# Kernel optimization log

Hardware: AMD Instinct MI355X
Metric: run time of the kernel (lower is better)

## Reference

```python
import jax, jax.numpy as jnp
import numpy as np

B = 128        # graphs per batch
N = 512        # nodes per graph (all graphs full-size)
F = 128        # input/hidden feature dim
DEG_AVG = 16   # average degree
E = B * N * DEG_AVG
DEGREES = (3, 3)  # polynomial filter order per conv layer


def setup_inputs() -> dict:
    key = jax.random.key(0)
    ks = jax.random.split(key, 8)
    X = jax.random.normal(ks[0], (B * N, F), dtype=jnp.float32)
    batch = jnp.repeat(jnp.arange(B, dtype=jnp.int32), N)
    # edges constrained within each graph: graph id = e // (N*DEG_AVG)
    gid = jnp.repeat(jnp.arange(B, dtype=jnp.int32), N * DEG_AVG)
    src = jax.random.randint(ks[1], (E,), 0, N, dtype=jnp.int32) + gid * N
    dst = jax.random.randint(ks[2], (E,), 0, N, dtype=jnp.int32) + gid * N
    edge_index = jnp.stack([src, dst], axis=0)
    s = 1.0 / np.sqrt(F)
    W1 = jax.random.normal(ks[3], (F, F), dtype=jnp.float32) * s
    b1 = jnp.zeros((F,), dtype=jnp.float32)
    W2 = jax.random.normal(ks[4], (F, F), dtype=jnp.float32) * s
    b2 = jnp.zeros((F,), dtype=jnp.float32)
    Wr1 = jax.random.normal(ks[5], (F, 64), dtype=jnp.float32) * s
    br1 = jnp.zeros((64,), dtype=jnp.float32)
    Wr2 = jax.random.normal(ks[6], (64, 1), dtype=jnp.float32) * (1.0 / 8.0)
    br2 = jnp.zeros((1,), dtype=jnp.float32)
    return {"X": X, "batch": batch, "edge_index": edge_index,
            "W1": W1, "b1": b1, "W2": W2, "b2": b2,
            "Wr1": Wr1, "br1": br1, "Wr2": Wr2, "br2": br2}


def _build_gso(edge_index):
    # dense per-graph adjacency [B, N, N] (block-diagonal global GSO,
    # represented batched for efficiency)
    g = edge_index[0] // N
    si = edge_index[0] % N
    di = edge_index[1] % N
    A = jnp.zeros((B, N, N), dtype=jnp.float32).at[g, si, di].set(1.0)
    # gso_generator: symmetric degree-normalized adjacency D^-1/2 A D^-1/2
    deg = A.sum(axis=-1)
    dinv = jnp.where(deg > 0, jax.lax.rsqrt(jnp.maximum(deg, 1e-12)), 0.0)
    S = dinv[:, :, None] * A * dinv[:, None, :]
    return S


def _poly_conv(S, x, degree, W, b):
    # sum_{k=0..degree} S^k x, then linear projection
    acc = x
    z = x
    for _ in range(degree):
        z = jnp.einsum('bij,bjf->bif', S, z)
        acc = acc + z
    return jnp.einsum('bnf,fo->bno', acc, W) + b


def reference(X, batch, edge_index, W1, b1, W2, b2, Wr1, br1, Wr2, br2):
    S = _build_gso(edge_index)
    x = X.reshape(B, N, F)  # nodes grouped per graph (batch is sorted)
    x = jax.nn.relu(_poly_conv(S, x, DEGREES[0], W1, b1))
    x = jax.nn.relu(_poly_conv(S, x, DEGREES[1], W2, b2))
    # global mean pool over nodes of each graph
    h = x.mean(axis=1)  # [B, F]
    h = jax.nn.relu(h @ Wr1 + br1)
    out = (h @ Wr2 + br2).squeeze(-1)  # [B]
    return out
```

## Files before the change

kernel.cpp:

```cpp
#include <hip/hip_runtime.h>
#include <hip/hip_bf16.h>

#define NB 128
#define NN 512
#define NF 128
#define BN (NB*NN)
#define NE (BN*16)
#define EPG 8192
#define WPR 16
#define ELLW 64
#define QST 40
#define SST 72
#define WTS 136

typedef short sh8 __attribute__((ext_vector_type(8)));
typedef float f32x4 __attribute__((ext_vector_type(4)));

static __device__ __forceinline__ unsigned short f2bf(float f) {
    unsigned u = __float_as_uint(f);
    u += 0x7fffu + ((u >> 16) & 1u);
    return (unsigned short)(u >> 16);
}

#define DOT2LO(acc_, pk_, one_) \
    asm("v_dot2_f32_bf16 %0, %1, %2, %0" : "+v"(acc_) : "v"(pk_), "v"(one_))

__global__ __launch_bounds__(512) void build_ell_fused_kernel(
    const int* __restrict__ src, const int* __restrict__ dst,
    unsigned short* __restrict__ ell, int* __restrict__ ocnt,
    float* __restrict__ dinvr, int* __restrict__ perm)
{
    __shared__ unsigned bm[NN * WPR];
    __shared__ int cs[NN];
    __shared__ int rdeg[NN];
    __shared__ int irank[NN];
    int g = blockIdx.x;
    int t = threadIdx.x;

    for (int i = t; i < NN * WPR; i += 512) bm[i] = 0u;
    __syncthreads();

    const int4* sg4 = (const int4*)(src + (size_t)g * EPG);
    const int4* dg4 = (const int4*)(dst + (size_t)g * EPG);
    for (int i = t; i < EPG / 4; i += 512) {
        int4 s4 = sg4[i];
        int4 d4 = dg4[i];
        int s, d;
        s = s4.x & (NN - 1); d = d4.x & (NN - 1);
        atomicOr(&bm[s * WPR + (d >> 5)], 1u << (d & 31));
        s = s4.y & (NN - 1); d = d4.y & (NN - 1);
        atomicOr(&bm[s * WPR + (d >> 5)], 1u << (d & 31));
        s = s4.z & (NN - 1); d = d4.z & (NN - 1);
        atomicOr(&bm[s * WPR + (d >> 5)], 1u << (d & 31));
        s = s4.w & (NN - 1); d = d4.w & (NN - 1);
        atomicOr(&bm[s * WPR + (d >> 5)], 1u << (d & 31));
    }
    __syncthreads();

    unsigned rw[WPR];
    #pragma unroll
    for (int w = 0; w < WPR; ++w) rw[w] = bm[t * WPR + w];
    int deg = 0;
    #pragma unroll
    for (int w = 0; w < WPR; ++w) deg += __popc(rw[w]);
    if (deg > ELLW) deg = ELLW;
    cs[t] = deg;
    __syncthreads();

    int rk = 0;
    for (int i = 0; i < NN; ++i) {
        int di_ = cs[i];
        rk += (di_ < deg) || (di_ == deg && i < t);
    }
    rdeg[rk] = deg;
    irank[t] = rk;
    perm[(size_t)g * NN + rk] = t;
    dinvr[(size_t)g * NN + rk] = (deg > 0) ? rsqrtf((float)deg) : 0.0f;
    __syncthreads();

    if (t < NN / 8) {
        int m = rdeg[t * 8 + 7];
        ocnt[(size_t)g * (NN / 8) + t] = (m + 3) & ~3;
    }

    unsigned short* els = (unsigned short*)bm;
    for (int qtr = 0; qtr < 4; ++qtr) {
        if ((rk >> 7) == qtr) {
            unsigned short* er = &els[(rk & 127) * SST];
            int c = 0;
            #pragma unroll
            for (int w = 0; w < WPR; ++w) {
                unsigned bits = rw[w];
                while (bits) {
                    int j = __ffs(bits) - 1;
                    bits &= bits - 1;
                    if (c < ELLW) er[c] = (unsigned short)irank[w * 32 + j];
                    ++c;
                }
            }
            if (c > ELLW) c = ELLW;
            for (int p = c; p < ELLW; ++p) er[p] = (unsigned short)NN;
        }
        __syncthreads();
        unsigned short* outb = ell + ((size_t)g * NN + qtr * 128) * ELLW;
        for (int idx = t; idx < 1024; idx += 512) {
            int r2 = idx >> 3, sg2 = idx & 7;
            uint4 v = *(const uint4*)&els[r2 * SST + sg2 * 8];
            *(uint4*)&outb[(size_t)r2 * ELLW + sg2 * 8] = v;
        }
        __syncthreads();
    }
}

__global__ __launch_bounds__(512, 4) void poly_fused_kernel(
    const float* __restrict__ xin,
    float* __restrict__ accout,
    const unsigned short* __restrict__ ell,
    const int* __restrict__ ocnt,
    const float* __restrict__ dinvr,
    const int* __restrict__ perm,
    int permuteIn)
{
    extern __shared__ float lds[];
    unsigned short* w = (unsigned short*)lds;
    float* dsh = lds + ((NN + 1) * QST * 2) / 4;

    int b = blockIdx.x;
    int g = b >> 2;
    int q = b & 3;
    int t = threadIdx.x;
    int lane = t & 63;
    int wid  = t >> 6;
    int slot = lane >> 2;
    int fb   = lane & 3;

    unsigned one_lo = 0x00003F80u;
    unsigned one_hi = 0x3F800000u;

    if (t < NN) dsh[t] = dinvr[(size_t)g * NN + t];
    if (t < QST) w[NN * QST + t] = 0;

    int rq0 = wid * 64;
    int rown = rq0 + slot;

    int px[4];
    if (permuteIn) {
        const int* pmg = perm + (size_t)g * NN + rown;
        #pragma unroll
        for (int x = 0; x < 4; ++x) px[x] = pmg[16 * x];
    } else {
        #pragma unroll
        for (int x = 0; x < 4; ++x) px[x] = rown + 16 * x;
    }

    const float* xg = xin + (size_t)g * NN * NF + q * 32 + fb * 8;

    float acc[4][8];
    #pragma unroll
    for (int x = 0; x < 4; ++x) {
        int row = px[x];
        float4 a0 = *(const float4*)&xg[(size_t)row * NF];
        float4 a1 = *(const float4*)&xg[(size_t)row * NF + 4];
        acc[x][0] = a0.x; acc[x][1] = a0.y; acc[x][2] = a0.z; acc[x][3] = a0.w;
        acc[x][4] = a1.x; acc[x][5] = a1.y; acc[x][6] = a1.z; acc[x][7] = a1.w;
    }

    const int* oc = ocnt + (((size_t)g * NN + rq0) >> 3);
    int co[4];
    #pragma unroll
    for (int x = 0; x < 4; ++x)
        co[x] = __builtin_amdgcn_readfirstlane(max(oc[2 * x], oc[2 * x + 1]));

    __syncthreads();

    #pragma unroll
    for (int x = 0; x < 4; ++x) {
        int rr = rown + 16 * x;
        float di = dsh[rr];
        unsigned pk[4];
        #pragma unroll
        for (int k = 0; k < 4; ++k) {
            unsigned lo = (unsigned)f2bf(di * acc[x][2 * k]);
            unsigned hi = (unsigned)f2bf(di * acc[x][2 * k + 1]);
            pk[k] = lo | (hi << 16);
        }
        *(uint4*)&w[rr * QST + fb * 8] = make_uint4(pk[0], pk[1], pk[2], pk[3]);
    }
    __syncthreads();

    const unsigned short* elbase = ell + ((size_t)g * NN + rown) * ELLW;

    for (int hop = 0; hop < 3; ++hop) {
        float stage[4][8];
        ushort4 nq = *(const ushort4*)elbase;
        #pragma unroll
        for (int x = 0; x < 4; ++x) {
            const unsigned short* el = elbase + (size_t)(16 * x) * ELLW;
            int cnt = co[x];
            ushort4 cur = nq;
            if (x < 3)
                nq = *(const ushort4*)(elbase + (size_t)(16 * (x + 1)) * ELLW);
            float s[8];
            #pragma unroll
            for (int k = 0; k < 8; ++k) s[k] = 0.0f;
            for (int p = 0; p < cnt; p += 4) {
                ushort4 nxt = cur;
                if (p + 4 < cnt) nxt = *(const ushort4*)(el + p + 4);
                uint4 v0 = *(const uint4*)&w[(int)cur.x * QST + fb * 8];
                uint4 v1 = *(const uint4*)&w[(int)cur.y * QST + fb * 8];
                uint4 v2 = *(const uint4*)&w[(int)cur.z * QST + fb * 8];
                uint4 v3 = *(const uint4*)&w[(int)cur.w * QST + fb * 8];
                unsigned d[4][4] = {{v0.x, v0.y, v0.z, v0.w},
                                    {v1.x, v1.y, v1.z, v1.w},
                                    {v2.x, v2.y, v2.z, v2.w},
                                    {v3.x, v3.y, v3.z, v3.w}};
                #pragma unroll
                for (int n = 0; n < 4; ++n) {
                    #pragma unroll
                    for (int k = 0; k < 4; ++k) {
                        DOT2LO(s[2 * k],     d[n][k], one_lo);
                        DOT2LO(s[2 * k + 1], d[n][k], one_hi);
                    }
                }
                cur = nxt;
            }
            #pragma unroll
            for (int k = 0; k < 8; ++k) stage[x][k] = s[k];
        }
        __syncthreads();
        #pragma unroll
        for (int x = 0; x < 4; ++x) {
            int rr = rown + 16 * x;
            float di = dsh[rr];
            unsigned pk[4];
            #pragma unroll
            for (int k = 0; k < 4; ++k) {
                float zlo = di * stage[x][2 * k];
                float zhi = di * stage[x][2 * k + 1];
                acc[x][2 * k]     += zlo;
                acc[x][2 * k + 1] += zhi;
                unsigned lo = (unsigned)f2bf(di * zlo);
                unsigned hi = (unsigned)f2bf(di * zhi);
                pk[k] = lo | (hi << 16);
            }
            *(uint4*)&w[rr * QST + fb * 8] = make_uint4(pk[0], pk[1], pk[2], pk[3]);
        }
        __syncthreads();
    }

    float* og = accout + (size_t)g * NN * NF + q * 32 + fb * 8;
    #pragma unroll
    for (int x = 0; x < 4; ++x) {
        int rr = rown + 16 * x;
        *(float4*)&og[(size_t)rr * NF] =
            make_float4(acc[x][0], acc[x][1], acc[x][2], acc[x][3]);
        *(float4*)&og[(size_t)rr * NF + 4] =
            make_float4(acc[x][4], acc[x][5], acc[x][6], acc[x][7]);
    }
}

__global__ __launch_bounds__(256, 2) void gemm_bias_relu_kernel(
    const float* __restrict__ X, const float* __restrict__ W,
    const float* __restrict__ b, float* __restrict__ Y,
    float* __restrict__ partial, int fuse)
{
    __shared__ __align__(16) unsigned short Wt[NF * WTS];
    __shared__ float part[4 * NF];

    int t = threadIdx.x;

    for (int i = t; i < NF * NF / 4; i += 256) {
        int k = i >> 5;
        int n4 = (i & 31) * 4;
        float4 wv = ((const float4*)W)[i];
        Wt[(n4 + 0) * WTS + k] = f2bf(wv.x);
        Wt[(n4 + 1) * WTS + k] = f2bf(wv.y);
        Wt[(n4 + 2) * WTS + k] = f2bf(wv.z);
        Wt[(n4 + 3) * WTS + k] = f2bf(wv.w);
    }
    __syncthreads();

    int lane = t & 63;
    int wid  = t >> 6;
    int quad = lane >> 4;
    int l16  = lane & 15;
    int rowA0 = blockIdx.x * 128 + wid * 32;

    union { unsigned short u[8]; sh8 v; } af[2][4];
    #pragma unroll
    for (int m = 0; m < 2; ++m) {
        int r = rowA0 + m * 16 + l16;
        const float* xr = X + (size_t)r * NF + quad * 8;
        #pragma unroll
        for (int kk = 0; kk < 4; ++kk) {
            float4 x0 = *(const float4*)(xr + kk * 32);
            float4 x1 = *(const float4*)(xr + kk * 32 + 4);
            af[m][kk].u[0] = f2bf(x0.x); af[m][kk].u[1] = f2bf(x0.y);
            af[m][kk].u[2] = f2bf(x0.z); af[m][kk].u[3] = f2bf(x0.w);
            af[m][kk].u[4] = f2bf(x1.x); af[m][kk].u[5] = f2bf(x1.y);
            af[m][kk].u[6] = f2bf(x1.z); af[m][kk].u[7] = f2bf(x1.w);
        }
    }

    f32x4 acc[2][8];
    #pragma unroll
    for (int m = 0; m < 2; ++m)
        #pragma unroll
        for (int c = 0; c < 8; ++c) acc[m][c] = (f32x4){0.f, 0.f, 0.f, 0.f};

    #pragma unroll
    for (int c = 0; c < 8; ++c) {
        const unsigned short* wb = &Wt[(c * 16 + l16) * WTS + quad * 8];
        #pragma unroll
        for (int kk = 0; kk < 4; ++kk) {
            union { uint4 q; sh8 v; } bf_;
            bf_.q = *(const uint4*)(wb + kk * 32);
            acc[0][c] = __builtin_amdgcn_mfma_f32_16x16x32_bf16(
                af[0][kk].v, bf_.v, acc[0][c], 0, 0, 0);
            acc[1][c] = __builtin_amdgcn_mfma_f32_16x16x32_bf16(
                af[1][kk].v, bf_.v, acc[1][c], 0, 0, 0);
        }
    }

    float psum[8];
    #pragma unroll
    for (int c = 0; c < 8; ++c) psum[c] = 0.0f;

    #pragma unroll
    for (int c = 0; c < 8; ++c) {
        int col = c * 16 + l16;
        float bias = b[col];
        #pragma unroll
        for (int m = 0; m < 2; ++m) {
            #pragma unroll
            for (int reg = 0; reg < 4; ++reg) {
                int r = rowA0 + m * 16 + quad * 4 + reg;
                float v = fmaxf(acc[m][c][reg] + bias, 0.0f);
                Y[(size_t)r * NF + col] = v;
                psum[c] += v;
            }
        }
    }

    if (fuse) {
        #pragma unroll
        for (int c = 0; c < 8; ++c) {
            float v = psum[c];
            v += __shfl_xor(v, 16);
            v += __shfl_xor(v, 32);
            if (lane < 16) part[wid * NF + c * 16 + lane] = v;
        }
        __syncthreads();
        if (t < NF) {
            float s = part[t] + part[NF + t] + part[2 * NF + t]
                    + part[3 * NF + t];
            partial[(size_t)blockIdx.x * NF + t] = s;
        }
    }
}

__global__ __launch_bounds__(128) void readout_kernel(
    const float* __restrict__ partial,
    const float* __restrict__ Wr1, const float* __restrict__ br1,
    const float* __restrict__ Wr2, const float* __restrict__ br2,
    float* __restrict__ out)
{
    __shared__ float hsh[NF];
    __shared__ float r1[64];

    int g = blockIdx.x;
    int t = threadIdx.x;

    const float* pg = partial + (size_t)g * 4 * NF;
    float s = 0.0f;
    #pragma unroll
    for (int j = 0; j < 4; ++j) s += pg[j * NF + t];
    hsh[t] = s * (1.0f / (float)NN);
    __syncthreads();

    if (t < 64) {
        float a = br1[t];
        #pragma unroll 8
        for (int k = 0; k < NF; ++k) a += hsh[k] * Wr1[k * 64 + t];
        r1[t] = fmaxf(a, 0.0f);
    }
    __syncthreads();

    if (t < 64) {
        float v = r1[t] * Wr2[t];
        #pragma unroll
        for (int off = 32; off; off >>= 1) v += __shfl_down(v, off);
        if (t == 0) out[g] = v + br2[0];
    }
}

extern "C" void kernel_launch(void* const* d_in, const int* in_sizes, int n_in,
                              void* d_out, int out_size, void* d_ws, size_t ws_size,
                              hipStream_t stream)
{
    const float* X    = (const float*)d_in[0];
    const int*   ei   = (const int*)d_in[2];
    const float* W1   = (const float*)d_in[3];
    const float* b1   = (const float*)d_in[4];
    const float* W2   = (const float*)d_in[5];
    const float* b2   = (const float*)d_in[6];
    const float* Wr1  = (const float*)d_in[7];
    const float* br1  = (const float*)d_in[8];
    const float* Wr2  = (const float*)d_in[9];
    const float* br2  = (const float*)d_in[10];
    float* out = (float*)d_out;

    const int* src = ei;
    const int* dst = ei + NE;

    char* ws = (char*)d_ws;
    float*          dinvr   = (float*)(ws);
    int*            ocnt    = (int*)(ws + (size_t)256 * 1024);
    int*            perm    = (int*)(ws + (size_t)512 * 1024);
    float*          partial = (float*)(ws + (size_t)768 * 1024);
    unsigned short* ell     = (unsigned short*)(ws + (size_t)1024 * 1024);
    float*          buf0    = (float*)(ws + (size_t)16384 * 1024);
    float*          buf1    = (float*)(ws + (size_t)49152 * 1024);

    build_ell_fused_kernel<<<NB, 512, 0, stream>>>(src, dst, ell, ocnt, dinvr,
                                                   perm);

    const size_t LDSSZ = (size_t)(NN + 1) * QST * 2 + NN * 4;

    poly_fused_kernel<<<NB * 4, 512, LDSSZ, stream>>>(X, buf0, ell, ocnt,
                                                      dinvr, perm, 1);
    gemm_bias_relu_kernel<<<BN / 128, 256, 0, stream>>>(buf0, W1, b1, buf1,
                                                        partial, 0);

    poly_fused_kernel<<<NB * 4, 512, LDSSZ, stream>>>(buf1, buf0, ell, ocnt,
                                                      dinvr, perm, 0);
    gemm_bias_relu_kernel<<<BN / 128, 256, 0, stream>>>(buf0, W2, b2, buf1,
                                                        partial, 1);

    readout_kernel<<<NB, 128, 0, stream>>>(partial, Wr1, br1, Wr2, br2, out);
}
```

Before: 251.3 us.

## Rebalance row assignment across waves and reorder block-to-graph mapping in poly kernel

Rows are now assigned to waves in a mirrored pattern (wave w takes one chunk from the front half and one from the mirrored back half), which appears intended to even out neighbor-count work across waves when rows are sorted by degree. Block indexing changes so consecutive blocks cover different graphs for the same feature quarter. The LDS row stride drops from 40 to 32 shorts, removing padding at the risk of more bank conflicts. Per-hop results are packed into registers right after each row's accumulation instead of being staged as raw floats.

```diff
diff --git a/kernel.cpp b/kernel.cpp
--- a/kernel.cpp
+++ b/kernel.cpp
@@ -9,7 +9,7 @@
 #define EPG 8192
 #define WPR 16
 #define ELLW 64
-#define QST 40
+#define QST 32
 #define SST 72
 #define WTS 136
 
@@ -126,13 +126,12 @@
     float* dsh = lds + ((NN + 1) * QST * 2) / 4;
 
     int b = blockIdx.x;
-    int g = b >> 2;
-    int q = b & 3;
+    int g = b & 127;
+    int q = b >> 7;
     int t = threadIdx.x;
-    int lane = t & 63;
-    int wid  = t >> 6;
-    int slot = lane >> 2;
-    int fb   = lane & 3;
+    int wid = t >> 6;
+    int qd  = (t >> 2) & 15;
+    int fbq = t & 3;
 
     unsigned one_lo = 0x00003F80u;
     unsigned one_hi = 0x3F800000u;
@@ -140,20 +139,32 @@
     if (t < NN) dsh[t] = dinvr[(size_t)g * NN + t];
     if (t < QST) w[NN * QST + t] = 0;
 
-    int rq0 = wid * 64;
-    int rown = rq0 + slot;
+    int rnk[4];
+    #pragma unroll
+    for (int x = 0; x < 4; ++x) {
+        int wl = (x >= 2) ? (7 - wid) : wid;
+        rnk[x] = x * 128 + wl * 16 + qd;
+    }
+
+    const int* oc = ocnt + (size_t)g * (NN / 8);
+    int co[4];
+    #pragma unroll
+    for (int x = 0; x < 4; ++x) {
+        int ob = (rnk[x] - qd) >> 3;
+        co[x] = __builtin_amdgcn_readfirstlane(max(oc[ob], oc[ob + 1]));
+    }
 
     int px[4];
     if (permuteIn) {
-        const int* pmg = perm + (size_t)g * NN + rown;
-        #pragma unroll
-        for (int x = 0; x < 4; ++x) px[x] = pmg[16 * x];
+        const int* pmg = perm + (size_t)g * NN;
+        #pragma unroll
+        for (int x = 0; x < 4; ++x) px[x] = pmg[rnk[x]];
     } else {
         #pragma unroll
-        for (int x = 0; x < 4; ++x) px[x] = rown + 16 * x;
-    }
-
-    const float* xg = xin + (size_t)g * NN * NF + q * 32 + fb * 8;
+        for (int x = 0; x < 4; ++x) px[x] = rnk[x];
+    }
+
+    const float* xg = xin + (size_t)g * NN * NF + q * 32 + fbq * 8;
 
     float acc[4][8];
     #pragma unroll
@@ -165,18 +176,11 @@
         acc[x][4] = a1.x; acc[x][5] = a1.y; acc[x][6] = a1.z; acc[x][7] = a1.w;
     }
 
-    const int* oc = ocnt + (((size_t)g * NN + rq0) >> 3);
-    int co[4];
-    #pragma unroll
-    for (int x = 0; x < 4; ++x)
-        co[x] = __builtin_amdgcn_readfirstlane(max(oc[2 * x], oc[2 * x + 1]));
-
     __syncthreads();
 
     #pragma unroll
     for (int x = 0; x < 4; ++x) {
-        int rr = rown + 16 * x;
-        float di = dsh[rr];
+        float di = dsh[rnk[x]];
         unsigned pk[4];
         #pragma unroll
         for (int k = 0; k < 4; ++k) {
@@ -184,32 +188,29 @@
             unsigned hi = (unsigned)f2bf(di * acc[x][2 * k + 1]);
             pk[k] = lo | (hi << 16);
         }
-        *(uint4*)&w[rr * QST + fb * 8] = make_uint4(pk[0], pk[1], pk[2], pk[3]);
-    }
-    __syncthreads();
-
-    const unsigned short* elbase = ell + ((size_t)g * NN + rown) * ELLW;
+        *(uint4*)&w[rnk[x] * QST + fbq * 8] = make_uint4(pk[0], pk[1], pk[2], pk[3]);
+    }
+    __syncthreads();
 
     for (int hop = 0; hop < 3; ++hop) {
-        float stage[4][8];
-        ushort4 nq = *(const ushort4*)elbase;
+        unsigned pst[4][4];
         #pragma unroll
         for (int x = 0; x < 4; ++x) {
-            const unsigned short* el = elbase + (size_t)(16 * x) * ELLW;
+            const unsigned short* el =
+                ell + ((size_t)g * NN + rnk[x]) * ELLW;
             int cnt = co[x];
-            ushort4 cur = nq;
-            if (x < 3)
-                nq = *(const ushort4*)(elbase + (size_t)(16 * (x + 1)) * ELLW);
             float s[8];
             #pragma unroll
             for (int k = 0; k < 8; ++k) s[k] = 0.0f;
+
+            ushort4 cur = *(const ushort4*)el;
             for (int p = 0; p < cnt; p += 4) {
                 ushort4 nxt = cur;
                 if (p + 4 < cnt) nxt = *(const ushort4*)(el + p + 4);
-                uint4 v0 = *(const uint4*)&w[(int)cur.x * QST + fb * 8];
-                uint4 v1 = *(const uint4*)&w[(int)cur.y * QST + fb * 8];
-                uint4 v2 = *(const uint4*)&w[(int)cur.z * QST + fb * 8];
-                uint4 v3 = *(const uint4*)&w[(int)cur.w * QST + fb * 8];
+                uint4 v0 = *(const uint4*)&w[(int)cur.x * QST + fbq * 8];
+                uint4 v1 = *(const uint4*)&w[(int)cur.y * QST + fbq * 8];
+                uint4 v2 = *(const uint4*)&w[(int)cur.z * QST + fbq * 8];
+                uint4 v3 = *(const uint4*)&w[(int)cur.w * QST + fbq * 8];
                 unsigned d[4][4] = {{v0.x, v0.y, v0.z, v0.w},
                                     {v1.x, v1.y, v1.z, v1.w},
                                     {v2.x, v2.y, v2.z, v2.w},
@@ -224,34 +225,32 @@
                 }
                 cur = nxt;
             }
-            #pragma unroll
-            for (int k = 0; k < 8; ++k) stage[x][k] = s[k];
-        }
-        __syncthreads();
-        #pragma unroll
-        for (int x = 0; x < 4; ++x) {
-            int rr = rown + 16 * x;
-            float di = dsh[rr];
-            unsigned pk[4];
+
+            float di = dsh[rnk[x]];
             #pragma unroll
             for (int k = 0; k < 4; ++k) {
-                float zlo = di * stage[x][2 * k];
-                float zhi = di * stage[x][2 * k + 1];
+                float zlo = di * s[2 * k];
+                float zhi = di * s[2 * k + 1];
                 acc[x][2 * k]     += zlo;
                 acc[x][2 * k + 1] += zhi;
                 unsigned lo = (unsigned)f2bf(di * zlo);
                 unsigned hi = (unsigned)f2bf(di * zhi);
-                pk[k] = lo | (hi << 16);
+                pst[x][k] = lo | (hi << 16);
             }
-            *(uint4*)&w[rr * QST + fb * 8] = make_uint4(pk[0], pk[1], pk[2], pk[3]);
         }
         __syncthreads();
-    }
-
-    float* og = accout + (size_t)g * NN * NF + q * 32 + fb * 8;
+        #pragma unroll
+        for (int x = 0; x < 4; ++x) {
+            *(uint4*)&w[rnk[x] * QST + fbq * 8] =
+                make_uint4(pst[x][0], pst[x][1], pst[x][2], pst[x][3]);
+        }
+        __syncthreads();
+    }
+
+    float* og = accout + (size_t)g * NN * NF + q * 32 + fbq * 8;
     #pragma unroll
     for (int x = 0; x < 4; ++x) {
-        int rr = rown + 16 * x;
+        int rr = rnk[x];
         *(float4*)&og[(size_t)rr * NF] =
             make_float4(acc[x][0], acc[x][1], acc[x][2], acc[x][3]);
         *(float4*)&og[(size_t)rr * NF + 4] =
```

Result: faster. 246.3 us (-2.0%).
